# Kernel tuning notes

Measured on AMD Instinct MI355X. Metric: run time of the kernel, lower is better.

## Reference

```python
import jax, jax.numpy as jnp
import numpy as np

B, DIM, H, W = 4, 192, 256, 256
HEADS, DS = 6, 2
CPH = DIM // HEADS  # channels per head = 32
DN = ('NCHW', 'OIHW', 'NCHW')


def _conv(x, w, padding, groups=1):
    return jax.lax.conv_general_dilated(x, w, (1, 1), padding,
                                        dimension_numbers=DN,
                                        feature_group_count=groups)


def setup_inputs() -> dict:
    key = jax.random.key(0)
    ks = jax.random.split(key, 5)
    x = jax.random.normal(ks[0], (B, DIM, H, W), dtype=jnp.float32)
    temperature = jnp.ones((HEADS, 1, 1), dtype=jnp.float32)
    qkv_w = jax.random.normal(ks[1], (3 * DIM, DIM, 1, 1), dtype=jnp.float32) * 0.02
    dw_w = jax.random.normal(ks[2], (3 * DIM, 1, 3, 3), dtype=jnp.float32) * 0.02
    proj_w = jax.random.normal(ks[3], (DIM, DIM, 1, 1), dtype=jnp.float32) * 0.02
    a = jnp.full((1,), 0.2, dtype=jnp.float32)
    return {"x": x, "temperature": temperature, "qkv_w": qkv_w, "dw_w": dw_w,
            "proj_w": proj_w, "a1": a, "a2": a, "a3": a, "a4": a}


def _masked_softmax(attn, kk):
    # top-k mask per row (exact torch.topk + scatter_ semantics)
    _, idx = jax.lax.top_k(attn, kk)                      # [b,h,C,kk]
    mask = jax.nn.one_hot(idx, attn.shape[-1], dtype=jnp.bool_).any(axis=-2)
    return jax.nn.softmax(jnp.where(mask, attn, -jnp.inf), axis=-1)


def reference(x, temperature, qkv_w, dw_w, proj_w, a1, a2, a3, a4):
    b, c, h, w = x.shape
    h2, w2 = h // DS, w // DS
    # 1x1 qkv conv at full res, then exact adaptive (regular) max pool by DS
    qkv = _conv(x, qkv_w, 'VALID')                        # [b, 3*dim, h, w]
    qkv = jax.lax.reduce_window(qkv, -jnp.inf, jax.lax.max,
                                (1, 1, DS, DS), (1, 1, DS, DS), 'VALID')
    # depthwise 3x3
    qkv = _conv(qkv, dw_w, 'SAME', groups=3 * DIM)        # [b, 3*dim, h2, w2]
    q, k, v = jnp.split(qkv, 3, axis=1)
    n = h2 * w2
    q = q.reshape(b, HEADS, CPH, n)
    k = k.reshape(b, HEADS, CPH, n)
    v = v.reshape(b, HEADS, CPH, n)
    # F.normalize along last dim (eps clamp 1e-12)
    q = q / jnp.maximum(jnp.linalg.norm(q, axis=-1, keepdims=True), 1e-12)
    k = k / jnp.maximum(jnp.linalg.norm(k, axis=-1, keepdims=True), 1e-12)
    attn = jnp.einsum('bhcn,bhdn->bhcd', q, k) * temperature[None]  # [b,h,C,C]
    Cc = attn.shape[-1]
    att1 = _masked_softmax(attn, Cc // 2)
    att2 = _masked_softmax(attn, Cc * 2 // 3)
    att3 = _masked_softmax(attn, Cc * 3 // 4)
    att4 = _masked_softmax(attn, Cc * 4 // 5)
    def apply(a):
        return jnp.einsum('bhcd,bhdn->bhcn', a, v)
    out = apply(att1) * a1 + apply(att2) * a2 + apply(att3) * a3 + apply(att4) * a4
    out = out.reshape(b, DIM, h2, w2)
    out = jax.nn.gelu(out, approximate=False)
    # nearest upsample by integer factor DS
    out = jnp.repeat(jnp.repeat(out, DS, axis=2), DS, axis=3)
    out = _conv(out, proj_w, 'VALID')
    return out
```

## Files before the change

kernel.cpp:

```cpp
#include <hip/hip_runtime.h>
#include <hip/hip_bf16.h>
#include <math.h>

typedef __attribute__((ext_vector_type(8))) short bf16x8;
typedef __attribute__((ext_vector_type(4))) float f32x4;
typedef __attribute__((ext_vector_type(4))) unsigned int u32x4;

#define NP 16384
#define HWFULL 65536

__device__ __forceinline__ unsigned short f2bf(float f){
    union { float f; unsigned int u; } v; v.f = f;
    unsigned int u = v.u;
    u += 0x7fffu + ((u >> 16) & 1u);
    return (unsigned short)(u >> 16);
}
__device__ __forceinline__ float bf2f(unsigned short h){
    union { unsigned int u; float f; } v; v.u = ((unsigned int)h) << 16;
    return v.f;
}
__device__ __forceinline__ unsigned int pk2(float a, float b){
    unsigned int r;
    asm("v_cvt_pk_bf16_f32 %0, %1, %2" : "=v"(r) : "v"(a), "v"(b));
    return r;
}

__global__ void k_convert2(const float* __restrict__ qw, const float* __restrict__ pw,
                           unsigned short* __restrict__ Wbf, unsigned short* __restrict__ Pbf){
    int i = blockIdx.x * 256 + threadIdx.x;
    if (i < 110592) Wbf[i] = f2bf(qw[i]);
    else if (i < 110592 + 36864) Pbf[i - 110592] = f2bf(pw[i - 110592]);
}

__global__ __launch_bounds__(256, 2)
void k_qkvpool(const float* __restrict__ x, const unsigned short* __restrict__ Wbf,
               unsigned short* __restrict__ qkvp){
    __shared__ unsigned short Bl[128*200];
    __shared__ unsigned short Ep[192*36];
    int tid = threadIdx.x;
    int lane = tid & 63, wv = tid >> 6;
    int n16 = lane & 15, quad = lane >> 4;
    int bx = blockIdx.x;
    int y2 = bx >> 2, x2blk = bx & 3;
    int b = blockIdx.y;

    #pragma unroll 6
    for (int j=0;j<12;j++){
        int idx = tid + j*256;
        int g = idx >> 7, w = idx & 127;
        int y = y2*2 + (w >> 6);
        int xc = x2blk*64 + (w & 63);
        const float* xp = x + (size_t)(b*192 + g*8) * HWFULL + y*256 + xc;
        float v0 = xp[0];
        float v1 = xp[(size_t)1*HWFULL];
        float v2 = xp[(size_t)2*HWFULL];
        float v3 = xp[(size_t)3*HWFULL];
        float v4 = xp[(size_t)4*HWFULL];
        float v5 = xp[(size_t)5*HWFULL];
        float v6 = xp[(size_t)6*HWFULL];
        float v7 = xp[(size_t)7*HWFULL];
        u32x4 pk;
        pk.x = pk2(v0,v1); pk.y = pk2(v2,v3); pk.z = pk2(v4,v5); pk.w = pk2(v6,v7);
        *(u32x4*)&Bl[w*200 + g*8] = pk;
    }
    bf16x8 afc[3], afn[3];
    #pragma unroll
    for (int j=0;j<3;j++)
        afc[j] = *(const bf16x8*)(Wbf + (size_t)(((wv*3+j)*16 + n16)*192 + quad*8));
    __syncthreads();

    for (int ocblk=0; ocblk<3; ocblk++){
        f32x4 acc[3][8];
        #pragma unroll
        for (int j=0;j<3;j++)
          #pragma unroll
          for (int s=0;s<8;s++)
            acc[j][s] = (f32x4){0.f,0.f,0.f,0.f};

        #pragma unroll 1
        for (int it=0; it<6; it++){
            int nocb = (it==5) ? ocblk+1 : ocblk;
            int nit  = (it==5) ? 0 : it+1;
            if (nocb < 3){
                #pragma unroll
                for (int j=0;j<3;j++)
                    afn[j] = *(const bf16x8*)(Wbf +
                        (size_t)((nocb*192 + (wv*3+j)*16 + n16)*192 + nit*32 + quad*8));
            }
            int bko = it*32 + quad*8;
            bf16x8 bfr[8];
            #pragma unroll
            for (int s=0;s<8;s++) bfr[s] = *(const bf16x8*)&Bl[(s*16 + n16)*200 + bko];
            #pragma unroll
            for (int j=0;j<3;j++)
              #pragma unroll
              for (int s=0;s<8;s++)
                acc[j][s] = __builtin_amdgcn_mfma_f32_16x16x32_bf16(afc[j], bfr[s], acc[j][s], 0,0,0);
            #pragma unroll
            for (int j=0;j<3;j++) afc[j] = afn[j];
        }
        __syncthreads();
        #pragma unroll
        for (int j=0;j<3;j++){
            int ocr = (wv*3+j)*16 + quad*4;
            #pragma unroll
            for (int sp=0;sp<4;sp++){
                #pragma unroll
                for (int r=0;r<4;r++){
                    float v = fmaxf(acc[j][sp][r], acc[j][sp+4][r]);
                    float o = __shfl_xor(v, 1, 64);
                    v = fmaxf(v, o);
                    if ((n16 & 1) == 0)
                        Ep[(ocr + r)*36 + sp*8 + (n16 >> 1)] = f2bf(v);
                }
            }
        }
        __syncthreads();
        size_t rowbase = (size_t)(b*576 + ocblk*192)*NP + y2*128 + x2blk*32;
        #pragma unroll
        for (int it2=0; it2<6; it2++){
            int c = tid + it2*256;
            int row = c >> 3, seg = c & 7;
            uint2 vv = *(const uint2*)&Ep[row*36 + seg*4];
            *(uint2*)(qkvp + rowbase + (size_t)row*NP + seg*4) = vv;
        }
    }
}

__global__ __launch_bounds__(256) void k_dwconv(const unsigned short* __restrict__ qkvp,
                                                const float* __restrict__ dww,
                                                unsigned short* __restrict__ dwoutB,
                                                float* __restrict__ sumsq){
    __shared__ unsigned short sl[128*128];
    __shared__ float wr[4];
    int tid = threadIdx.x;
    int ch = blockIdx.x, b = blockIdx.y;
    const unsigned short* in = qkvp + (size_t)(b*576 + ch)*NP;
    #pragma unroll
    for (int j=0;j<8;j++){
        int idx = tid + j*256;
        *(u32x4*)&sl[idx*8] = *(const u32x4*)(in + idx*8);
    }
    float w0 = dww[ch*9+0], w1 = dww[ch*9+1], w2 = dww[ch*9+2];
    float w3 = dww[ch*9+3], w4 = dww[ch*9+4], w5 = dww[ch*9+5];
    float w6 = dww[ch*9+6], w7 = dww[ch*9+7], w8 = dww[ch*9+8];
    __syncthreads();
    int c = tid & 127, half = tid >> 7;
    float mL = (c > 0) ? 1.f : 0.f, mR = (c < 127) ? 1.f : 0.f;
    int cm = (c > 0) ? c-1 : c, cp = (c < 127) ? c+1 : c;
    unsigned short* outp = dwoutB + (size_t)(b*576 + ch)*NP;
    float ssq = 0.f;
    int r0 = half*64;
    float r0a, r0b, r0c, r1a, r1b, r1c;
    if (half == 0){ r0a = r0b = r0c = 0.f; }
    else { int rr = r0-1;
           r0a = bf2f(sl[rr*128+cm])*mL; r0b = bf2f(sl[rr*128+c]); r0c = bf2f(sl[rr*128+cp])*mR; }
    { int rr = r0;
      r1a = bf2f(sl[rr*128+cm])*mL; r1b = bf2f(sl[rr*128+c]); r1c = bf2f(sl[rr*128+cp])*mR; }
    #pragma unroll 4
    for (int i=0;i<64;i++){
        int rr = r0 + i + 1;
        float r2a, r2b, r2c;
        if (rr < 128){
            r2a = bf2f(sl[rr*128+cm])*mL; r2b = bf2f(sl[rr*128+c]); r2c = bf2f(sl[rr*128+cp])*mR;
        } else { r2a = r2b = r2c = 0.f; }
        float a = r0a*w0 + r0b*w1 + r0c*w2
                + r1a*w3 + r1b*w4 + r1c*w5
                + r2a*w6 + r2b*w7 + r2c*w8;
        outp[(r0+i)*128 + c] = (unsigned short)pk2(a, a);
        ssq += a*a;
        r0a=r1a; r0b=r1b; r0c=r1c;
        r1a=r2a; r1b=r2b; r1c=r2c;
    }
    if (ch < 384){
        #pragma unroll
        for (int off=32; off>0; off>>=1) ssq += __shfl_down(ssq, off, 64);
        if ((tid & 63) == 0) wr[tid >> 6] = ssq;
        __syncthreads();
        if (tid == 0) sumsq[b*384 + ch] = wr[0] + wr[1] + wr[2] + wr[3];
    }
}

__global__ __launch_bounds__(256) void k_attnraw(const unsigned short* __restrict__ dwoutB,
                                                 float* __restrict__ attn){
    __shared__ unsigned short sq[32*264];
    __shared__ unsigned short sk[32*264];
    __shared__ float red[4][32][33];
    int tid = threadIdx.x;
    int lane = tid & 63, wv = tid >> 6;
    int n16 = lane & 15, quad = lane >> 4;
    int h = blockIdx.y, b = blockIdx.z;
    int n0 = blockIdx.x * 256;
    const unsigned short* qb = dwoutB + (size_t)(b*576 + h*32)*NP + n0;
    const unsigned short* kb = dwoutB + (size_t)(b*576 + 192 + h*32)*NP + n0;

    #pragma unroll
    for (int j=0;j<4;j++){
        int idx = tid + j*256;
        int row = idx >> 5, seg = idx & 31;
        *(u32x4*)&sq[row*264 + seg*8] = *(const u32x4*)(qb + (size_t)row*NP + seg*8);
        *(u32x4*)&sk[row*264 + seg*8] = *(const u32x4*)(kb + (size_t)row*NP + seg*8);
    }
    __syncthreads();

    f32x4 acc[2][2];
    #pragma unroll
    for (int i=0;i<2;i++)
      #pragma unroll
      for (int j=0;j<2;j++) acc[i][j] = (f32x4){0.f,0.f,0.f,0.f};

    #pragma unroll
    for (int ks=0; ks<2; ks++){
        int ko = wv*64 + ks*32 + quad*8;
        bf16x8 aq0 = *(const bf16x8*)&sq[n16*264 + ko];
        bf16x8 aq1 = *(const bf16x8*)&sq[(16+n16)*264 + ko];
        bf16x8 bk0 = *(const bf16x8*)&sk[n16*264 + ko];
        bf16x8 bk1 = *(const bf16x8*)&sk[(16+n16)*264 + ko];
        acc[0][0] = __builtin_amdgcn_mfma_f32_16x16x32_bf16(aq0, bk0, acc[0][0], 0,0,0);
        acc[0][1] = __builtin_amdgcn_mfma_f32_16x16x32_bf16(aq0, bk1, acc[0][1], 0,0,0);
        acc[1][0] = __builtin_amdgcn_mfma_f32_16x16x32_bf16(aq1, bk0, acc[1][0], 0,0,0);
        acc[1][1] = __builtin_amdgcn_mfma_f32_16x16x32_bf16(aq1, bk1, acc[1][1], 0,0,0);
    }
    #pragma unroll
    for (int cc=0; cc<2; cc++)
      #pragma unroll
      for (int dd=0; dd<2; dd++)
        #pragma unroll
        for (int r=0; r<4; r++)
          red[wv][cc*16 + quad*4 + r][dd*16 + n16] = acc[cc][dd][r];
    __syncthreads();
    float* ap = attn + (size_t)(b*6+h)*1024;
    #pragma unroll
    for (int j=0;j<4;j++){
        int o = tid + j*256;
        int c = o >> 5, d = o & 31;
        float v = red[0][c][d] + red[1][c][d] + red[2][c][d] + red[3][c][d];
        atomicAdd(ap + o, v);
    }
}

__global__ void k_mask_softmax(const float* __restrict__ attn, const float* __restrict__ sumsq,
                               const float* __restrict__ temp,
                               const float* __restrict__ A1, const float* __restrict__ A2,
                               const float* __restrict__ A3, const float* __restrict__ A4,
                               float* __restrict__ comb){
    __shared__ float Am[32][33];
    __shared__ float qn[32], kn[32];
    int t = threadIdx.x;
    int bh = blockIdx.x;
    int b = bh / 6, h = bh % 6;
    if (t < 32) qn[t] = fmaxf(sqrtf(sumsq[b*384 + h*32 + t]), 1e-12f);
    else if (t >= 64 && t < 96) kn[t-64] = fmaxf(sqrtf(sumsq[b*384 + 192 + h*32 + (t-64)]), 1e-12f);
    __syncthreads();
    int c = t >> 5, d = t & 31;
    float tv = temp[h];
    float am = attn[(size_t)bh*1024 + t] * tv / (qn[c]*kn[d]);
    Am[c][d] = am;
    float m = am;
    #pragma unroll
    for (int off=16; off>0; off>>=1) m = fmaxf(m, __shfl_down(m, off, 32));
    m = __shfl(m, 0, 32);
    float e = expf(am - m);
    __syncthreads();
    int rk = 0;
    #pragma unroll 8
    for (int dd=0; dd<32; dd++){
        float av = Am[c][dd];
        rk += (av > am) || (av == am && dd < d);
    }
    float e0 = rk < 16 ? e : 0.f;
    float e1 = rk < 21 ? e : 0.f;
    float e2 = rk < 24 ? e : 0.f;
    float e3 = rk < 25 ? e : 0.f;
    #pragma unroll
    for (int off=16; off>0; off>>=1){
        e0 += __shfl_down(e0, off, 32);
        e1 += __shfl_down(e1, off, 32);
        e2 += __shfl_down(e2, off, 32);
        e3 += __shfl_down(e3, off, 32);
    }
    float d0 = __shfl(e0, 0, 32), d1 = __shfl(e1, 0, 32);
    float d2 = __shfl(e2, 0, 32), d3 = __shfl(e3, 0, 32);
    float s = (rk<16 ? A1[0]/d0 : 0.f) + (rk<21 ? A2[0]/d1 : 0.f)
            + (rk<24 ? A3[0]/d2 : 0.f) + (rk<25 ? A4[0]/d3 : 0.f);
    comb[(size_t)bh*1024 + t] = e * s;
}

__global__ __launch_bounds__(256, 2)
void k_avproj(const unsigned short* __restrict__ dwoutB, const float* __restrict__ comb,
              const unsigned short* __restrict__ Pbf, float* __restrict__ out){
    __shared__ unsigned short Bl[128*200];
    __shared__ float cm[6144];
    int tid = threadIdx.x;
    int y2 = blockIdx.x, b = blockIdx.y;

    #pragma unroll
    for (int j=0;j<24;j++) cm[tid + j*256] = comb[b*6144 + tid + j*256];

    int n_loc = tid & 127, half = tid >> 7;
    const unsigned short* vb = dwoutB + (size_t)(b*576 + 384 + half*96)*NP + y2*128 + n_loc;
    __syncthreads();
    #pragma unroll 1
    for (int hh=0; hh<3; hh++){
        float v[32];
        #pragma unroll
        for (int d=0; d<32; d++) v[d] = bf2f(vb[(size_t)(hh*32+d)*NP]);
        const float* chp = &cm[(half*3+hh)*1024];
        #pragma unroll 1
        for (int cg=0; cg<4; cg++){
            float s[8];
            #pragma unroll
            for (int i=0;i<8;i++){
                const float* crow = chp + (cg*8+i)*32;
                float acc = 0.f;
                #pragma unroll
                for (int d=0;d<32;d++) acc += crow[d]*v[d];
                s[i] = 0.5f*acc*(1.f + erff(acc*0.70710678118654752f));
            }
            u32x4 pk;
            pk.x = pk2(s[0],s[1]); pk.y = pk2(s[2],s[3]);
            pk.z = pk2(s[4],s[5]); pk.w = pk2(s[6],s[7]);
            *(u32x4*)&Bl[n_loc*200 + half*96 + hh*32 + cg*8] = pk;
        }
    }

    int lane = tid & 63, wv = tid >> 6;
    int n16 = lane & 15, quad = lane >> 4;
    bf16x8 afc[3], afn[3];
    #pragma unroll
    for (int j=0;j<3;j++)
        afc[j] = *(const bf16x8*)(Pbf + (size_t)(((wv*3+j)*16 + n16)*192 + quad*8));
    __syncthreads();

    f32x4 acc[3][8];
    #pragma unroll
    for (int j=0;j<3;j++)
      #pragma unroll
      for (int s=0;s<8;s++)
        acc[j][s] = (f32x4){0.f,0.f,0.f,0.f};

    #pragma unroll 1
    for (int it=0; it<6; it++){
        if (it < 5){
            #pragma unroll
            for (int j=0;j<3;j++)
                afn[j] = *(const bf16x8*)(Pbf +
                    (size_t)(((wv*3+j)*16 + n16)*192 + (it+1)*32 + quad*8));
        }
        int bko = it*32 + quad*8;
        bf16x8 bfr[8];
        #pragma unroll
        for (int s=0;s<8;s++) bfr[s] = *(const bf16x8*)&Bl[(s*16 + n16)*200 + bko];
        #pragma unroll
        for (int j=0;j<3;j++)
          #pragma unroll
          for (int s=0;s<8;s++)
            acc[j][s] = __builtin_amdgcn_mfma_f32_16x16x32_bf16(afc[j], bfr[s], acc[j][s], 0,0,0);
        #pragma unroll
        for (int j=0;j<3;j++) afc[j] = afn[j];
    }

    #pragma unroll
    for (int j=0;j<3;j++){
        int oc = (wv*3+j)*16 + quad*4;
        #pragma unroll
        for (int sp=0;sp<8;sp++){
            int x2 = sp*16 + n16;
            #pragma unroll
            for (int r=0;r<4;r++){
                float v = acc[j][sp][r];
                size_t o = ((size_t)(b*192 + oc + r)*256 + 2*y2)*256 + 2*x2;
                float2 val = make_float2(v, v);
                *(float2*)(out + o) = val;
                *(float2*)(out + o + 256) = val;
            }
        }
    }
}

extern "C" void kernel_launch(void* const* d_in, const int* in_sizes, int n_in,
                              void* d_out, int out_size, void* d_ws, size_t ws_size,
                              hipStream_t stream){
    const float* x     = (const float*)d_in[0];
    const float* temp  = (const float*)d_in[1];
    const float* qkvw  = (const float*)d_in[2];
    const float* dww   = (const float*)d_in[3];
    const float* projw = (const float*)d_in[4];
    const float* A1    = (const float*)d_in[5];
    const float* A2    = (const float*)d_in[6];
    const float* A3    = (const float*)d_in[7];
    const float* A4    = (const float*)d_in[8];
    float* out = (float*)d_out;
    char* ws = (char*)d_ws;

    unsigned short* dwoutB = (unsigned short*)ws;
    unsigned short* qkvp   = (unsigned short*)(ws + 75497472ull);
    unsigned short* Wbf    = (unsigned short*)(ws + 150994944ull);
    unsigned short* Pbf    = (unsigned short*)(ws + 151216128ull);
    float*          attn   = (float*)(ws + 151289856ull);
    float*          comb   = (float*)(ws + 151388160ull);
    float*          sumsq  = (float*)(ws + 151486464ull);

    hipMemsetAsync(attn, 0, 98304, stream);
    k_convert2<<<dim3((147456+255)/256), dim3(256), 0, stream>>>(qkvw, projw, Wbf, Pbf);
    k_qkvpool<<<dim3(512,4), dim3(256), 0, stream>>>(x, Wbf, qkvp);
    k_dwconv<<<dim3(576,4), dim3(256), 0, stream>>>(qkvp, dww, dwoutB, sumsq);
    k_attnraw<<<dim3(64,6,4), dim3(256), 0, stream>>>(dwoutB, attn);
    k_mask_softmax<<<dim3(24), dim3(1024), 0, stream>>>(attn, sumsq, temp, A1, A2, A3, A4, comb);
    k_avproj<<<dim3(128,4), dim3(256), 0, stream>>>(dwoutB, comb, Pbf, out);
}
```

Measured before the change: 522.0 us.

## Fuse q/k depthwise conv into Gram kernel, keep separate dwconv for v

The depthwise 3x3 conv for the q and k channels is now computed inside the attention Gram kernel, straight from the pooled qkv buffer into shared memory. This drops the bf16 write and reread of q/k through global memory. Only the v channels still go through a standalone depthwise kernel. Sum-of-squares is now gathered with atomics, which needs an extra memset. Each thread recomputes halo rows from global memory with 34-wide register arrays, so reads overlap and register pressure rises.

```diff
diff --git a/kernel.cpp b/kernel.cpp
--- a/kernel.cpp
+++ b/kernel.cpp
@@ -127,29 +127,135 @@
     }
 }
 
-__global__ __launch_bounds__(256) void k_dwconv(const unsigned short* __restrict__ qkvp,
+__global__ __launch_bounds__(256) void k_qkgram(const unsigned short* __restrict__ qkvp,
                                                 const float* __restrict__ dww,
-                                                unsigned short* __restrict__ dwoutB,
+                                                float* __restrict__ attn,
                                                 float* __restrict__ sumsq){
+    __shared__ unsigned short sq[32*264];
+    __shared__ unsigned short sk[32*264];
+    __shared__ float red[4][32][33];
+    int tid = threadIdx.x;
+    int h = blockIdx.y, b = blockIdx.z;
+    int y0 = blockIdx.x * 2;
+    int cc = tid >> 2, sub = tid & 3;
+    int chg = (cc < 32) ? (h*32 + cc) : (192 + h*32 + (cc - 32));
+    const unsigned short* img = qkvp + (size_t)(b*576 + chg)*NP;
+    float w[9];
+    #pragma unroll
+    for (int i=0;i<9;i++) w[i] = dww[chg*9 + i];
+    unsigned short* dst = (cc < 32) ? sq : sk;
+    int ccl = cc & 31;
+    float ssq = 0.f;
+
+    #pragma unroll 1
+    for (int tt=0; tt<2; tt++){
+        int st = sub*2 + tt;
+        int r01 = st >> 2, qtr = st & 3;
+        int y = y0 + r01;
+        int x0 = qtr*32;
+        float acc[32];
+        #pragma unroll
+        for (int i=0;i<32;i++) acc[i] = 0.f;
+        #pragma unroll
+        for (int dy=0; dy<3; dy++){
+            int ry = y - 1 + dy;
+            float rowf[34];
+            if (ry >= 0 && ry < 128){
+                const unsigned short* rp = img + ry*128 + x0;
+                rowf[0] = (x0 > 0) ? bf2f(rp[-1]) : 0.f;
+                #pragma unroll
+                for (int j=0;j<4;j++){
+                    bf16x8 v = *(const bf16x8*)(rp + j*8);
+                    #pragma unroll
+                    for (int i=0;i<8;i++) rowf[1 + j*8 + i] = bf2f((unsigned short)v[i]);
+                }
+                rowf[33] = (x0 + 32 < 128) ? bf2f(rp[32]) : 0.f;
+            } else {
+                #pragma unroll
+                for (int i=0;i<34;i++) rowf[i] = 0.f;
+            }
+            float wa = w[dy*3], wb = w[dy*3+1], wc = w[dy*3+2];
+            #pragma unroll
+            for (int i=0;i<32;i++)
+                acc[i] += wa*rowf[i] + wb*rowf[i+1] + wc*rowf[i+2];
+        }
+        unsigned short* drow = dst + ccl*264 + r01*128 + x0;
+        #pragma unroll
+        for (int g8=0; g8<4; g8++){
+            u32x4 pk;
+            pk.x = pk2(acc[g8*8+0], acc[g8*8+1]);
+            pk.y = pk2(acc[g8*8+2], acc[g8*8+3]);
+            pk.z = pk2(acc[g8*8+4], acc[g8*8+5]);
+            pk.w = pk2(acc[g8*8+6], acc[g8*8+7]);
+            *(u32x4*)(drow + g8*8) = pk;
+        }
+        #pragma unroll
+        for (int i=0;i<32;i++) ssq += acc[i]*acc[i];
+    }
+    ssq += __shfl_down(ssq, 1, 64);
+    ssq += __shfl_down(ssq, 2, 64);
+    if (sub == 0) atomicAdd(&sumsq[b*384 + chg], ssq);
+    __syncthreads();
+
+    int lane = tid & 63, wv = tid >> 6;
+    int n16 = lane & 15, quad = lane >> 4;
+    f32x4 gac[2][2];
+    #pragma unroll
+    for (int i=0;i<2;i++)
+      #pragma unroll
+      for (int j=0;j<2;j++) gac[i][j] = (f32x4){0.f,0.f,0.f,0.f};
+
+    #pragma unroll
+    for (int ks=0; ks<2; ks++){
+        int ko = wv*64 + ks*32 + quad*8;
+        bf16x8 aq0 = *(const bf16x8*)&sq[n16*264 + ko];
+        bf16x8 aq1 = *(const bf16x8*)&sq[(16+n16)*264 + ko];
+        bf16x8 bk0 = *(const bf16x8*)&sk[n16*264 + ko];
+        bf16x8 bk1 = *(const bf16x8*)&sk[(16+n16)*264 + ko];
+        gac[0][0] = __builtin_amdgcn_mfma_f32_16x16x32_bf16(aq0, bk0, gac[0][0], 0,0,0);
+        gac[0][1] = __builtin_amdgcn_mfma_f32_16x16x32_bf16(aq0, bk1, gac[0][1], 0,0,0);
+        gac[1][0] = __builtin_amdgcn_mfma_f32_16x16x32_bf16(aq1, bk0, gac[1][0], 0,0,0);
+        gac[1][1] = __builtin_amdgcn_mfma_f32_16x16x32_bf16(aq1, bk1, gac[1][1], 0,0,0);
+    }
+    #pragma unroll
+    for (int cc2=0; cc2<2; cc2++)
+      #pragma unroll
+      for (int dd=0; dd<2; dd++)
+        #pragma unroll
+        for (int r=0; r<4; r++)
+          red[wv][cc2*16 + quad*4 + r][dd*16 + n16] = gac[cc2][dd][r];
+    __syncthreads();
+    float* ap = attn + (size_t)(b*6+h)*1024;
+    #pragma unroll
+    for (int j=0;j<4;j++){
+        int o = tid + j*256;
+        int c = o >> 5, d = o & 31;
+        float v = red[0][c][d] + red[1][c][d] + red[2][c][d] + red[3][c][d];
+        atomicAdd(ap + o, v);
+    }
+}
+
+__global__ __launch_bounds__(256) void k_dwv(const unsigned short* __restrict__ qkvp,
+                                             const float* __restrict__ dww,
+                                             unsigned short* __restrict__ dwoutB){
     __shared__ unsigned short sl[128*128];
-    __shared__ float wr[4];
     int tid = threadIdx.x;
-    int ch = blockIdx.x, b = blockIdx.y;
-    const unsigned short* in = qkvp + (size_t)(b*576 + ch)*NP;
+    int chg = 384 + blockIdx.x;
+    int b = blockIdx.y;
+    const unsigned short* in = qkvp + (size_t)(b*576 + chg)*NP;
     #pragma unroll
     for (int j=0;j<8;j++){
         int idx = tid + j*256;
         *(u32x4*)&sl[idx*8] = *(const u32x4*)(in + idx*8);
     }
-    float w0 = dww[ch*9+0], w1 = dww[ch*9+1], w2 = dww[ch*9+2];
-    float w3 = dww[ch*9+3], w4 = dww[ch*9+4], w5 = dww[ch*9+5];
-    float w6 = dww[ch*9+6], w7 = dww[ch*9+7], w8 = dww[ch*9+8];
+    float w0 = dww[chg*9+0], w1 = dww[chg*9+1], w2 = dww[chg*9+2];
+    float w3 = dww[chg*9+3], w4 = dww[chg*9+4], w5 = dww[chg*9+5];
+    float w6 = dww[chg*9+6], w7 = dww[chg*9+7], w8 = dww[chg*9+8];
     __syncthreads();
     int c = tid & 127, half = tid >> 7;
     float mL = (c > 0) ? 1.f : 0.f, mR = (c < 127) ? 1.f : 0.f;
     int cm = (c > 0) ? c-1 : c, cp = (c < 127) ? c+1 : c;
-    unsigned short* outp = dwoutB + (size_t)(b*576 + ch)*NP;
-    float ssq = 0.f;
+    unsigned short* outp = dwoutB + (size_t)(b*576 + chg)*NP;
     int r0 = half*64;
     float r0a, r0b, r0c, r1a, r1b, r1c;
     if (half == 0){ r0a = r0b = r0c = 0.f; }
@@ -167,75 +273,9 @@
         float a = r0a*w0 + r0b*w1 + r0c*w2
                 + r1a*w3 + r1b*w4 + r1c*w5
                 + r2a*w6 + r2b*w7 + r2c*w8;
-        outp[(r0+i)*128 + c] = (unsigned short)pk2(a, a);
-        ssq += a*a;
+        outp[(r0+i)*128 + c] = f2bf(a);
         r0a=r1a; r0b=r1b; r0c=r1c;
         r1a=r2a; r1b=r2b; r1c=r2c;
-    }
-    if (ch < 384){
-        #pragma unroll
-        for (int off=32; off>0; off>>=1) ssq += __shfl_down(ssq, off, 64);
-        if ((tid & 63) == 0) wr[tid >> 6] = ssq;
-        __syncthreads();
-        if (tid == 0) sumsq[b*384 + ch] = wr[0] + wr[1] + wr[2] + wr[3];
-    }
-}
-
-__global__ __launch_bounds__(256) void k_attnraw(const unsigned short* __restrict__ dwoutB,
-                                                 float* __restrict__ attn){
-    __shared__ unsigned short sq[32*264];
-    __shared__ unsigned short sk[32*264];
-    __shared__ float red[4][32][33];
-    int tid = threadIdx.x;
-    int lane = tid & 63, wv = tid >> 6;
-    int n16 = lane & 15, quad = lane >> 4;
-    int h = blockIdx.y, b = blockIdx.z;
-    int n0 = blockIdx.x * 256;
-    const unsigned short* qb = dwoutB + (size_t)(b*576 + h*32)*NP + n0;
-    const unsigned short* kb = dwoutB + (size_t)(b*576 + 192 + h*32)*NP + n0;
-
-    #pragma unroll
-    for (int j=0;j<4;j++){
-        int idx = tid + j*256;
-        int row = idx >> 5, seg = idx & 31;
-        *(u32x4*)&sq[row*264 + seg*8] = *(const u32x4*)(qb + (size_t)row*NP + seg*8);
-        *(u32x4*)&sk[row*264 + seg*8] = *(const u32x4*)(kb + (size_t)row*NP + seg*8);
-    }
-    __syncthreads();
-
-    f32x4 acc[2][2];
-    #pragma unroll
-    for (int i=0;i<2;i++)
-      #pragma unroll
-      for (int j=0;j<2;j++) acc[i][j] = (f32x4){0.f,0.f,0.f,0.f};
-
-    #pragma unroll
-    for (int ks=0; ks<2; ks++){
-        int ko = wv*64 + ks*32 + quad*8;
-        bf16x8 aq0 = *(const bf16x8*)&sq[n16*264 + ko];
-        bf16x8 aq1 = *(const bf16x8*)&sq[(16+n16)*264 + ko];
-        bf16x8 bk0 = *(const bf16x8*)&sk[n16*264 + ko];
-        bf16x8 bk1 = *(const bf16x8*)&sk[(16+n16)*264 + ko];
-        acc[0][0] = __builtin_amdgcn_mfma_f32_16x16x32_bf16(aq0, bk0, acc[0][0], 0,0,0);
-        acc[0][1] = __builtin_amdgcn_mfma_f32_16x16x32_bf16(aq0, bk1, acc[0][1], 0,0,0);
-        acc[1][0] = __builtin_amdgcn_mfma_f32_16x16x32_bf16(aq1, bk0, acc[1][0], 0,0,0);
-        acc[1][1] = __builtin_amdgcn_mfma_f32_16x16x32_bf16(aq1, bk1, acc[1][1], 0,0,0);
-    }
-    #pragma unroll
-    for (int cc=0; cc<2; cc++)
-      #pragma unroll
-      for (int dd=0; dd<2; dd++)
-        #pragma unroll
-        for (int r=0; r<4; r++)
-          red[wv][cc*16 + quad*4 + r][dd*16 + n16] = acc[cc][dd][r];
-    __syncthreads();
-    float* ap = attn + (size_t)(b*6+h)*1024;
-    #pragma unroll
-    for (int j=0;j<4;j++){
-        int o = tid + j*256;
-        int c = o >> 5, d = o & 31;
-        float v = red[0][c][d] + red[1][c][d] + red[2][c][d] + red[3][c][d];
-        atomicAdd(ap + o, v);
     }
 }
 
@@ -402,10 +442,11 @@
     float*          sumsq  = (float*)(ws + 151486464ull);
 
     hipMemsetAsync(attn, 0, 98304, stream);
+    hipMemsetAsync(sumsq, 0, 6144, stream);
     k_convert2<<<dim3((147456+255)/256), dim3(256), 0, stream>>>(qkvw, projw, Wbf, Pbf);
     k_qkvpool<<<dim3(512,4), dim3(256), 0, stream>>>(x, Wbf, qkvp);
-    k_dwconv<<<dim3(576,4), dim3(256), 0, stream>>>(qkvp, dww, dwoutB, sumsq);
-    k_attnraw<<<dim3(64,6,4), dim3(256), 0, stream>>>(dwoutB, attn);
+    k_qkgram<<<dim3(64,6,4), dim3(256), 0, stream>>>(qkvp, dww, attn, sumsq);
+    k_dwv<<<dim3(192,4), dim3(256), 0, stream>>>(qkvp, dww, dwoutB);
     k_mask_softmax<<<dim3(24), dim3(1024), 0, stream>>>(attn, sumsq, temp, A1, A2, A3, A4, comb);
     k_avproj<<<dim3(128,4), dim3(256), 0, stream>>>(dwoutB, comb, Pbf, out);
 }
```

New measurement: 530.1 us. About the same (+1.6%).
